# Kernel optimization log

Measured on AMD Instinct MI355X. Metric: run time of the kernel, lower is better.

Reference implementation:

```python
import jax, jax.numpy as jnp
import numpy as np

D_MODEL, D_K, D_V, N_HEADS = 1024, 64, 64, 16
B, S = 2, 2048
LN_EPS = 1e-5


def setup_inputs() -> dict:
    key = jax.random.key(0)
    ks = jax.random.split(key, 12)
    s = 1.0 / np.sqrt(D_MODEL)
    inp = {
        "Q": jax.random.normal(ks[0], (B, S, D_MODEL), jnp.float32),
        "K": jax.random.normal(ks[1], (B, S, D_MODEL), jnp.float32),
        "V": jax.random.normal(ks[2], (B, S, D_MODEL), jnp.float32),
        "attn_mask": jax.random.bernoulli(ks[3], 0.1, (B, S, S)),
        "Wq": jax.random.uniform(ks[4], (D_MODEL, D_K * N_HEADS), jnp.float32, -s, s),
        "bq": jnp.zeros((D_K * N_HEADS,), jnp.float32),
        "Wk": jax.random.uniform(ks[5], (D_MODEL, D_K * N_HEADS), jnp.float32, -s, s),
        "bk": jnp.zeros((D_K * N_HEADS,), jnp.float32),
        "Wv": jax.random.uniform(ks[6], (D_MODEL, D_V * N_HEADS), jnp.float32, -s, s),
        "bv": jnp.zeros((D_V * N_HEADS,), jnp.float32),
        "Wo": jax.random.uniform(ks[7], (N_HEADS * D_V, D_MODEL), jnp.float32, -s, s),
        "bo": jnp.zeros((D_MODEL,), jnp.float32),
        "gamma": jnp.ones((D_MODEL,), jnp.float32),
        "beta": jnp.zeros((D_MODEL,), jnp.float32),
    }
    return inp


def reference(Q, K, V, attn_mask, Wq, bq, Wk, bk, Wv, bv, Wo, bo, gamma, beta):
    b, s, _ = Q.shape
    # projections -> [B, S, H, d]
    q = (Q @ Wq + bq).reshape(b, s, N_HEADS, D_K)
    k = (K @ Wk + bk).reshape(b, -1, N_HEADS, D_K)
    v = (V @ Wv + bv).reshape(b, -1, N_HEADS, D_V)
    # scores [B, H, Sq, Sk]
    scores = jnp.einsum("bqhd,bkhd->bhqk", q, k) / np.sqrt(D_K).astype(np.float32)
    scores = jnp.where(attn_mask[:, None, :, :], jnp.float32(-1e9), scores)
    attn = jax.nn.softmax(scores, axis=-1)
    context = jnp.einsum("bhqk,bkhd->bqhd", attn, v).reshape(b, s, N_HEADS * D_V)
    out = context @ Wo + bo + Q  # residual
    mu = jnp.mean(out, axis=-1, keepdims=True)
    var = jnp.var(out, axis=-1, keepdims=True)
    return (out - mu) * jax.lax.rsqrt(var + LN_EPS) * gamma + beta
```

## Files before the change

kernel.cpp:

```cpp
#include <hip/hip_runtime.h>
#include <hip/hip_bf16.h>
#include <math.h>


#define D_MODEL 1024
#define NHEADS  16
#define DHEAD   64
#define BATCH   2
#define SEQ     2048
#define MROWS   (BATCH * SEQ)
#define SCLF    0.18033688f

typedef __attribute__((ext_vector_type(8)))  short bf16x8;
typedef __attribute__((ext_vector_type(4)))  float f32x4;
typedef __attribute__((ext_vector_type(16))) float f32x16;

__device__ inline unsigned short f2bf(float f) {
    unsigned int u = __builtin_bit_cast(unsigned int, f);
    unsigned int r = (u + 0x7FFFu + ((u >> 16) & 1u)) >> 16;
    return (unsigned short)r;
}

__device__ inline unsigned cvtpk_bf16(float lo, float hi2) {
    unsigned r;
    asm("v_cvt_pk_bf16_f32 %0, %1, %2" : "=v"(r) : "v"(lo), "v"(hi2));
    return r;
}

__device__ inline void gload16(const unsigned short* g, unsigned short* lbase, int lane) {
#if __has_builtin(__builtin_amdgcn_global_load_lds)
    __builtin_amdgcn_global_load_lds(
        (const __attribute__((address_space(1))) unsigned int*)g,
        (__attribute__((address_space(3))) unsigned int*)lbase, 16, 0, 0);
#else
    *(bf16x8*)(lbase + lane * 8) = *(const bf16x8*)g;
#endif
}

__global__ __launch_bounds__(256) void detect_mask_par(
    const unsigned int* __restrict__ m, int nwords, int* __restrict__ flags)
{
    const int i = blockIdx.x * 256 + threadIdx.x;
    int a = 0, b = 0;
    if (i < nwords) {
        const unsigned int w = m[i];
        a = (w != 0u && w != 1u);
        b = (w != 0u && w != 0x3F800000u);
    }
    const int wa = (int)__any(a);
    const int wb = (int)__any(b);
    if ((threadIdx.x & 63) == 0) {
        if (wa) atomicOr(&flags[0], 1);
        if (wb) atomicOr(&flags[1], 1);
    }
}

__global__ __launch_bounds__(256) void pack_mask_ballot(
    const void* __restrict__ mask, const int* __restrict__ flags,
    unsigned long long* __restrict__ mbits, int nwords)
{
    const int lane   = threadIdx.x & 63;
    const int wv     = blockIdx.x * 4 + (threadIdx.x >> 6);
    const int nwaves = gridDim.x * 4;
    const int mf = (flags[0] == 0) ? 0 : (flags[1] == 0) ? 1 : 2;
    for (int w = wv; w < nwords; w += nwaves) {
        bool bit;
        if (mf == 0)      bit = ((const unsigned int*)mask)[(size_t)w * 64 + lane] != 0u;
        else if (mf == 1) bit = ((const float*)mask)[(size_t)w * 64 + lane] != 0.f;
        else              bit = ((const unsigned char*)mask)[(size_t)w * 64 + lane] != 0;
        const unsigned long long b = __ballot(bit);
        if (lane == 0) mbits[w] = b;
    }
}

__global__ __launch_bounds__(256) void cvt_all(
    const float* __restrict__ Q, const float* __restrict__ K,
    const float* __restrict__ V,
    const float* __restrict__ w0, const float* __restrict__ w1,
    const float* __restrict__ w2, const float* __restrict__ w3,
    unsigned short* __restrict__ Qb, unsigned short* __restrict__ Kb,
    unsigned short* __restrict__ Vb,
    unsigned short* __restrict__ t0, unsigned short* __restrict__ t1,
    unsigned short* __restrict__ t2, unsigned short* __restrict__ t3)
{
    __shared__ float tile[64][65];
    const int z = blockIdx.z;
    if (z < 3) {
        const float* s = (z == 0) ? Q : (z == 1) ? K : V;
        unsigned short* d = (z == 0) ? Qb : (z == 1) ? Kb : Vb;
        const int i = blockIdx.x * 256 + threadIdx.x;
        float4 a = ((const float4*)s)[i * 2];
        float4 b = ((const float4*)s)[i * 2 + 1];
        unsigned u0 = cvtpk_bf16(a.x, a.y);
        unsigned u1 = cvtpk_bf16(a.z, a.w);
        unsigned u2 = cvtpk_bf16(b.x, b.y);
        unsigned u3 = cvtpk_bf16(b.z, b.w);
        ((int4*)d)[i] = make_int4((int)u0, (int)u1, (int)u2, (int)u3);
    } else {
        if (blockIdx.x >= 256) return;
        const int wz = z - 3;
        const float* W = (wz == 0) ? w0 : (wz == 1) ? w1 : (wz == 2) ? w2 : w3;
        unsigned short* T = (wz == 0) ? t0 : (wz == 1) ? t1 : (wz == 2) ? t2 : t3;
        const int n0 = (blockIdx.x & 15) * 64;
        const int k0 = (blockIdx.x >> 4) * 64;
        const int t  = threadIdx.x;
        const int r  = t >> 4;
        const int c4 = (t & 15) * 4;
        #pragma unroll
        for (int u = 0; u < 4; ++u) {
            float4 v = *(const float4*)(W + (size_t)(k0 + r + u * 16) * D_MODEL + n0 + c4);
            tile[r + u * 16][c4 + 0] = v.x;
            tile[r + u * 16][c4 + 1] = v.y;
            tile[r + u * 16][c4 + 2] = v.z;
            tile[r + u * 16][c4 + 3] = v.w;
        }
        __syncthreads();
        #pragma unroll
        for (int u = 0; u < 4; ++u) {
            const int nr = r + u * 16;
            ushort4 o;
            o.x = f2bf(tile[c4 + 0][nr]);
            o.y = f2bf(tile[c4 + 1][nr]);
            o.z = f2bf(tile[c4 + 2][nr]);
            o.w = f2bf(tile[c4 + 3][nr]);
            *(ushort4*)(T + (size_t)(n0 + nr) * D_MODEL + k0 + c4) = o;
        }
    }
}

#define BKQ 32
__global__ __launch_bounds__(256, 1) void gemm_qkv(
    const unsigned short* __restrict__ A0, const unsigned short* __restrict__ A1,
    const unsigned short* __restrict__ A2,
    const unsigned short* __restrict__ B0, const unsigned short* __restrict__ B1,
    const unsigned short* __restrict__ B2,
    const float* __restrict__ bias0, const float* __restrict__ bias1,
    const float* __restrict__ bias2,
    unsigned short* __restrict__ C0, unsigned short* __restrict__ C1,
    unsigned short* __restrict__ C2)
{
    const int z = blockIdx.z;
    const unsigned short* A  = (z == 0) ? A0 : (z == 1) ? A1 : A2;
    const unsigned short* Bt = (z == 0) ? B0 : (z == 1) ? B1 : B2;
    const float* bias        = (z == 0) ? bias0 : (z == 1) ? bias1 : bias2;
    unsigned short* C        = (z == 0) ? C0 : (z == 1) ? C1 : C2;
    const int K = D_MODEL, N = D_MODEL;

    __shared__ unsigned short As[2][128 * BKQ];
    __shared__ unsigned short Bs[2][128 * BKQ];
    const int tid  = threadIdx.x;
    const int w    = tid >> 6;
    const int lane = tid & 63;
    const int lo   = lane & 15;
    const int hi   = lane >> 4;
    const int wm   = (w >> 1) * 64;
    const int wn   = (w & 1) * 64;
    const int m0   = blockIdx.x * 128;
    const int n0   = blockIdx.y * 128;

    const unsigned short* Ab = A  + (size_t)m0 * K;
    const unsigned short* Bb = Bt + (size_t)n0 * K;

    f32x4 acc[4][4];
    #pragma unroll
    for (int i = 0; i < 4; ++i)
        #pragma unroll
        for (int j = 0; j < 4; ++j) acc[i][j] = (f32x4){0.f, 0.f, 0.f, 0.f};

    const int NT = K / BKQ;
    auto stage = [&](int buf, int t) {
        const int k0 = t * BKQ;
        #pragma unroll
        for (int i = 0; i < 2; ++i) {
            const int c = i * 256 + tid;
            gload16(Ab + (size_t)(c >> 2) * K + k0 + (c & 3) * 8,
                    &As[buf][(i * 256 + w * 64) * 8], lane);
        }
        #pragma unroll
        for (int i = 0; i < 2; ++i) {
            const int c = i * 256 + tid;
            gload16(Bb + (size_t)(c >> 2) * K + k0 + (c & 3) * 8,
                    &Bs[buf][(i * 256 + w * 64) * 8], lane);
        }
    };

    stage(0, 0);
    __syncthreads();
    int cur = 0;
    for (int t = 0; t < NT; ++t) {
        if (t + 1 < NT) stage(cur ^ 1, t + 1);
        bf16x8 af[4], bfr[4];
        #pragma unroll
        for (int f = 0; f < 4; ++f) {
            af[f]  = *(const bf16x8*)&As[cur][(wm + f * 16 + lo) * BKQ + hi * 8];
            bfr[f] = *(const bf16x8*)&Bs[cur][(wn + f * 16 + lo) * BKQ + hi * 8];
        }
        #pragma unroll
        for (int fm = 0; fm < 4; ++fm)
            #pragma unroll
            for (int fn = 0; fn < 4; ++fn)
                acc[fm][fn] = __builtin_amdgcn_mfma_f32_16x16x32_bf16(
                    af[fm], bfr[fn], acc[fm][fn], 0, 0, 0);
        __syncthreads();
        cur ^= 1;
    }

    #pragma unroll
    for (int fm = 0; fm < 4; ++fm) {
        const int row = m0 + wm + fm * 16 + hi * 4;
        #pragma unroll
        for (int fn = 0; fn < 4; ++fn) {
            const int col = n0 + wn + fn * 16 + lo;
            const float bv = bias[col];
            #pragma unroll
            for (int r = 0; r < 4; ++r) {
                float o = acc[fm][fn][r] + bv;
                if (z == 0) o *= SCLF;
                if (z < 2)
                    C[(size_t)(row + r) * N + col] = f2bf(o);
                else
                    C[(size_t)((row + r) >> 11) * 2097152
                      + (size_t)col * 2048 + ((row + r) & 2047)] = f2bf(o);
            }
        }
    }
}

#define BKK 64
__global__ __launch_bounds__(256) void gemm_out64(
    const unsigned short* __restrict__ A, const unsigned short* __restrict__ Bt,
    const float* __restrict__ bias, const float* __restrict__ resid,
    float* __restrict__ C)
{
    const int K = D_MODEL, N = D_MODEL;
    __shared__ unsigned short As[2][128 * BKK];
    __shared__ unsigned short Bs[2][64 * BKK];
    const int tid  = threadIdx.x;
    const int w    = tid >> 6;
    const int lane = tid & 63;
    const int lo   = lane & 15;
    const int hi   = lane >> 4;
    const int wm   = (w >> 1) * 64;
    const int wn   = (w & 1) * 32;
    const int m0   = blockIdx.x * 128;
    const int n0   = blockIdx.y * 64;

    const unsigned short* Ab = A  + (size_t)m0 * K;
    const unsigned short* Bb = Bt + (size_t)n0 * K;

    f32x4 acc[4][2];
    #pragma unroll
    for (int i = 0; i < 4; ++i)
        #pragma unroll
        for (int j = 0; j < 2; ++j) acc[i][j] = (f32x4){0.f, 0.f, 0.f, 0.f};

    const int NT = K / BKK;
    auto stage = [&](int buf, int t) {
        const int k0 = t * BKK;
        #pragma unroll
        for (int i = 0; i < 4; ++i) {
            const int c = i * 256 + tid;
            gload16(Ab + (size_t)(c >> 3) * K + k0 + (c & 7) * 8,
                    &As[buf][(i * 256 + w * 64) * 8], lane);
        }
        #pragma unroll
        for (int i = 0; i < 2; ++i) {
            const int c = i * 256 + tid;
            gload16(Bb + (size_t)(c >> 3) * K + k0 + (c & 7) * 8,
                    &Bs[buf][(i * 256 + w * 64) * 8], lane);
        }
    };

    stage(0, 0);
    __syncthreads();
    int cur = 0;
    for (int t = 0; t < NT; ++t) {
        if (t + 1 < NT) stage(cur ^ 1, t + 1);
        bf16x8 af[4][2], bfr[2][2];
        #pragma unroll
        for (int f = 0; f < 4; ++f)
            #pragma unroll
            for (int s = 0; s < 2; ++s)
                af[f][s] = *(const bf16x8*)&As[cur][(wm + f * 16 + lo) * BKK + s * 32 + hi * 8];
        #pragma unroll
        for (int f = 0; f < 2; ++f)
            #pragma unroll
            for (int s = 0; s < 2; ++s)
                bfr[f][s] = *(const bf16x8*)&Bs[cur][(wn + f * 16 + lo) * BKK + s * 32 + hi * 8];
        #pragma unroll
        for (int s = 0; s < 2; ++s)
            #pragma unroll
            for (int fm = 0; fm < 4; ++fm)
                #pragma unroll
                for (int fn = 0; fn < 2; ++fn)
                    acc[fm][fn] = __builtin_amdgcn_mfma_f32_16x16x32_bf16(
                        af[fm][s], bfr[fn][s], acc[fm][fn], 0, 0, 0);
        __syncthreads();
        cur ^= 1;
    }

    #pragma unroll
    for (int fm = 0; fm < 4; ++fm) {
        const int row = m0 + wm + fm * 16 + hi * 4;
        #pragma unroll
        for (int fn = 0; fn < 2; ++fn) {
            const int col = n0 + wn + fn * 16 + lo;
            const float bv = bias[col];
            #pragma unroll
            for (int r = 0; r < 4; ++r)
                C[(size_t)(row + r) * N + col] =
                    acc[fm][fn][r] + bv + resid[(size_t)(row + r) * N + col];
        }
    }
}

__global__ __launch_bounds__(512, 2) void attn_mfma32(
    const unsigned short* __restrict__ qb, const unsigned short* __restrict__ kbm,
    const unsigned short* __restrict__ vt,
    const unsigned long long* __restrict__ mbits, unsigned short* __restrict__ ctx)
{
    __shared__ unsigned char smem[65536];
    const int tid  = threadIdx.x;
    const int w8   = tid >> 6;
    const int g    = w8 >> 2;
    const int wq   = w8 & 3;
    const int lane = tid & 63;
    const int l31  = lane & 31;
    const int hi   = lane >> 5;
    const int h    = blockIdx.x;
    const int q0   = blockIdx.y * 128;
    const int b    = blockIdx.z;

    unsigned short* KsG = (unsigned short*)smem + (size_t)g * 8192;
    unsigned short* VsG = (unsigned short*)(smem + 32768) + (size_t)g * 8192;

    const size_t qkbase = (size_t)b * SEQ * D_MODEL + (size_t)h * DHEAD;
    const size_t vtbase = ((size_t)b * D_MODEL + h * DHEAD) * SEQ;

    const int qtok = q0 + wq * 32 + l31;
    bf16x8 qA[4];
    #pragma unroll
    for (int s = 0; s < 4; ++s)
        qA[s] = *(const bf16x8*)(qb + qkbase + (size_t)qtok * D_MODEL + s * 16 + hi * 8);

    f32x16 o0 = {}, o1 = {};
    float l_i = 0.f;

    const unsigned long long* mrow = mbits + ((size_t)b * SEQ + qtok) * (SEQ / 64);

    const int srow = lane >> 3;
    const int sc   = lane & 7;
    const int r0   = wq * 16 + srow;
    const int swz  = sc ^ (r0 & 7);

    const unsigned short* kl0 = kbm + qkbase + (size_t)(g * 1024 + r0) * D_MODEL + swz * 8;
    const unsigned short* kl1 = kl0 + (size_t)8 * D_MODEL;
    const unsigned short* vl0 = vt + vtbase + (size_t)r0 * SEQ + g * 1024 + swz * 8;
    const unsigned short* vl1 = vl0 + (size_t)8 * SEQ;
    const int ldk0 = (wq * 16) * 64;
    const int ldk1 = (wq * 16 + 8) * 64;

    auto stage = [&](int buf) {
        gload16(kl0, &KsG[buf * 4096 + ldk0], lane);
        gload16(kl1, &KsG[buf * 4096 + ldk1], lane);
        gload16(vl0, &VsG[buf * 4096 + ldk0], lane);
        gload16(vl1, &VsG[buf * 4096 + ldk1], lane);
        kl0 += (size_t)64 * D_MODEL;
        kl1 += (size_t)64 * D_MODEL;
        vl0 += 64;
        vl1 += 64;
    };

    stage(0);
    unsigned long long mw64 = mrow[g * 16];
    __syncthreads();
    int cur = 0;

    for (int t = 0; t < 16; ++t) {
        if (t + 1 < 16) stage(cur ^ 1);
        const unsigned long long mwc = mw64;
        if (t + 1 < 16) mw64 = mrow[g * 16 + t + 1];
        const unsigned int ml = (unsigned int)(mwc >> (4 * hi));
        const unsigned int mh = (unsigned int)(mwc >> (32 + 4 * hi));

        f32x16 st0 = {}, st1 = {};
        __builtin_amdgcn_s_setprio(1);
        #pragma unroll
        for (int s = 0; s < 4; ++s) {
            bf16x8 kf0 = *(const bf16x8*)&KsG[cur * 4096 + l31 * 64 + ((2 * s + hi) ^ (l31 & 7)) * 8];
            st0 = __builtin_amdgcn_mfma_f32_32x32x16_bf16(kf0, qA[s], st0, 0, 0, 0);
            bf16x8 kf1 = *(const bf16x8*)&KsG[cur * 4096 + (32 + l31) * 64 + ((2 * s + hi) ^ (l31 & 7)) * 8];
            st1 = __builtin_amdgcn_mfma_f32_32x32x16_bf16(kf1, qA[s], st1, 0, 0, 0);
        }
        __builtin_amdgcn_s_setprio(0);

        float sp[4] = {0.f, 0.f, 0.f, 0.f};
        #pragma unroll
        for (int r = 0; r < 16; ++r) {
            const int klo = (r & 3) + 8 * (r >> 2);
            const float x0 = ((ml >> klo) & 1u) ? -1e9f : st0[r];
            const float x1 = ((mh >> klo) & 1u) ? -1e9f : st1[r];
            const float e0 = exp2f(x0);
            const float e1 = exp2f(x1);
            st0[r] = e0; st1[r] = e1;
            sp[r & 3] += e0 + e1;
        }
        l_i += (sp[0] + sp[1]) + (sp[2] + sp[3]);

        bf16x8 pa[4];
        #pragma unroll
        for (int s = 0; s < 4; ++s) {
            const int base = (s & 1) * 8;
            unsigned av, bv2, cv, dv;
            if (s < 2) {
                av  = cvtpk_bf16(st0[base + 0], st0[base + 1]);
                bv2 = cvtpk_bf16(st0[base + 4], st0[base + 5]);
                cv  = cvtpk_bf16(st0[base + 2], st0[base + 3]);
                dv  = cvtpk_bf16(st0[base + 6], st0[base + 7]);
            } else {
                av  = cvtpk_bf16(st1[base + 0], st1[base + 1]);
                bv2 = cvtpk_bf16(st1[base + 4], st1[base + 5]);
                cv  = cvtpk_bf16(st1[base + 2], st1[base + 3]);
                dv  = cvtpk_bf16(st1[base + 6], st1[base + 7]);
            }
            asm("v_permlane32_swap_b32 %0, %1" : "+v"(av), "+v"(bv2));
            asm("v_permlane32_swap_b32 %0, %1" : "+v"(cv), "+v"(dv));
            int4 pk = make_int4((int)av, (int)cv, (int)bv2, (int)dv);
            pa[s] = __builtin_bit_cast(bf16x8, pk);
        }

        __builtin_amdgcn_s_setprio(1);
        #pragma unroll
        for (int s = 0; s < 4; ++s) {
            bf16x8 vf0 = *(const bf16x8*)&VsG[cur * 4096 + l31 * 64 + ((2 * s + hi) ^ (l31 & 7)) * 8];
            o0 = __builtin_amdgcn_mfma_f32_32x32x16_bf16(pa[s], vf0, o0, 0, 0, 0);
            bf16x8 vf1 = *(const bf16x8*)&VsG[cur * 4096 + (32 + l31) * 64 + ((2 * s + hi) ^ (l31 & 7)) * 8];
            o1 = __builtin_amdgcn_mfma_f32_32x32x16_bf16(pa[s], vf1, o1, 0, 0, 0);
        }
        __builtin_amdgcn_s_setprio(0);
        __syncthreads();
        cur ^= 1;
    }

    l_i += __shfl_xor(l_i, 32, 64);
    __syncthreads();
    float* comb = (float*)smem;
    if (g == 1) {
        float* p = comb + (size_t)(wq * 64 + lane) * 33;
        #pragma unroll
        for (int r = 0; r < 16; ++r) { p[r] = o0[r]; p[16 + r] = o1[r]; }
        p[32] = l_i;
    }
    __syncthreads();
    if (g == 0) {
        const float* p = comb + (size_t)(wq * 64 + lane) * 33;
        const float inv = 1.f / (l_i + p[32]);
        #pragma unroll
        for (int r = 0; r < 16; ++r) {
            const int qloc = (r & 3) + 8 * (r >> 2) + 4 * hi;
            const float ivr = __shfl(inv, qloc, 64);
            unsigned short* dst = ctx + qkbase + (size_t)(q0 + wq * 32 + qloc) * D_MODEL;
            dst[l31]      = f2bf((o0[r] + p[r]) * ivr);
            dst[32 + l31] = f2bf((o1[r] + p[16 + r]) * ivr);
        }
    }
}

__global__ __launch_bounds__(256) void layernorm1024(
    const float* __restrict__ x, const float* __restrict__ gamma,
    const float* __restrict__ beta, float* __restrict__ out)
{
    const int row = blockIdx.x;
    const int tid = threadIdx.x;
    const float* xr = x + (size_t)row * D_MODEL;
    float4 v = *(const float4*)(xr + (tid << 2));
    float s = v.x + v.y + v.z + v.w;
    float q = v.x * v.x + v.y * v.y + v.z * v.z + v.w * v.w;
    #pragma unroll
    for (int off = 1; off < 64; off <<= 1) {
        s += __shfl_xor(s, off, 64);
        q += __shfl_xor(q, off, 64);
    }
    __shared__ float sw[4], qw_[4];
    const int wid = tid >> 6;
    if ((tid & 63) == 0) { sw[wid] = s; qw_[wid] = q; }
    __syncthreads();
    s = sw[0] + sw[1] + sw[2] + sw[3];
    q = qw_[0] + qw_[1] + qw_[2] + qw_[3];
    const float mu  = s * (1.f / D_MODEL);
    const float var = q * (1.f / D_MODEL) - mu * mu;
    const float a = var + 1e-5f;
    float inv = rsqrtf(a);
    inv = inv * (1.5f - 0.5f * a * inv * inv);
    float4 gg = *(const float4*)(gamma + (tid << 2));
    float4 bt = *(const float4*)(beta + (tid << 2));
    float4 o;
    o.x = (v.x - mu) * inv * gg.x + bt.x;
    o.y = (v.y - mu) * inv * gg.y + bt.y;
    o.z = (v.z - mu) * inv * gg.z + bt.z;
    o.w = (v.w - mu) * inv * gg.w + bt.w;
    *(float4*)(out + (size_t)row * D_MODEL + (tid << 2)) = o;
}

extern "C" void kernel_launch(void* const* d_in, const int* in_sizes, int n_in,
                              void* d_out, int out_size, void* d_ws, size_t ws_size,
                              hipStream_t stream)
{
    const float* Q    = (const float*)d_in[0];
    const float* K    = (const float*)d_in[1];
    const float* V    = (const float*)d_in[2];
    const void*  mask = d_in[3];
    const float* Wq   = (const float*)d_in[4];
    const float* bq   = (const float*)d_in[5];
    const float* Wk   = (const float*)d_in[6];
    const float* bk   = (const float*)d_in[7];
    const float* Wv   = (const float*)d_in[8];
    const float* bv   = (const float*)d_in[9];
    const float* Wo   = (const float*)d_in[10];
    const float* bo   = (const float*)d_in[11];
    const float* gam  = (const float*)d_in[12];
    const float* bet  = (const float*)d_in[13];
    float* out = (float*)d_out;

    const size_t NE = (size_t)MROWS * D_MODEL;
    const size_t WE = (size_t)D_MODEL * D_MODEL;
    const size_t NMW = (size_t)BATCH * SEQ * (SEQ / 64);
    unsigned short* Qbf = (unsigned short*)d_ws;
    unsigned short* Kbf = Qbf + NE;
    unsigned short* Vbf = Kbf + NE;
    unsigned short* qb  = Vbf + NE;
    unsigned short* kb  = qb + NE;
    unsigned short* vt  = kb + NE;
    unsigned short* Wt0 = vt + NE;
    unsigned short* Wt1 = Wt0 + WE;
    unsigned short* Wt2 = Wt1 + WE;
    unsigned short* Wt3 = Wt2 + WE;
    unsigned long long* mbits = (unsigned long long*)(Wt3 + WE);
    int* mflags = (int*)(mbits + NMW);
    unsigned short* ctxb = Qbf;
    float* outp = (float*)Kbf;
    if (ws_size < 6 * NE * 2 + 4 * WE * 2 + NMW * 8 + 64) return;

    hipMemsetAsync(mflags, 0, 2 * sizeof(int), stream);
    detect_mask_par<<<256, 256, 0, stream>>>((const unsigned int*)mask, 65536, mflags);
    pack_mask_ballot<<<2048, 256, 0, stream>>>(mask, mflags, mbits, (int)NMW);

    cvt_all<<<dim3(2048, 1, 7), 256, 0, stream>>>(Q, K, V, Wq, Wk, Wv, Wo,
                                                  Qbf, Kbf, Vbf, Wt0, Wt1, Wt2, Wt3);

    gemm_qkv<<<dim3(32, 8, 3), 256, 0, stream>>>(Qbf, Kbf, Vbf, Wt0, Wt1, Wt2,
                                                 bq, bk, bv, qb, kb, vt);

    dim3 ag(NHEADS, SEQ / 128, BATCH);
    attn_mfma32<<<ag, 512, 0, stream>>>(qb, kb, vt, mbits, ctxb);

    gemm_out64<<<dim3(32, 16), 256, 0, stream>>>(ctxb, Wt3, bo, Q, outp);

    layernorm1024<<<MROWS, 256, 0, stream>>>(outp, gam, bet, out);
}
```

Before: 187.3 us.

## Halve attention KV tile to 32 keys to shrink LDS and registers

Cuts the per-iteration key/value tile in the attention kernel from 64 to 32 keys, doubling the loop trip count. Shared memory drops from 64KB to about 33KB, and the score accumulators and P fragments are halved. The K and V staging layouts and swizzles are reworked to fit the smaller tile. This is meant to lower LDS and register pressure so more blocks can be resident, at the cost of twice as many barriers and stage steps per pass with less MFMA work between them.

```diff
diff --git a/kernel.cpp b/kernel.cpp
--- a/kernel.cpp
+++ b/kernel.cpp
@@ -319,7 +319,7 @@
     const unsigned short* __restrict__ vt,
     const unsigned long long* __restrict__ mbits, unsigned short* __restrict__ ctx)
 {
-    __shared__ unsigned char smem[65536];
+    __shared__ __align__(16) unsigned char smem[33792];
     const int tid  = threadIdx.x;
     const int w8   = tid >> 6;
     const int g    = w8 >> 2;
@@ -331,8 +331,8 @@
     const int q0   = blockIdx.y * 128;
     const int b    = blockIdx.z;
 
-    unsigned short* KsG = (unsigned short*)smem + (size_t)g * 8192;
-    unsigned short* VsG = (unsigned short*)(smem + 32768) + (size_t)g * 8192;
+    unsigned short* KsG = (unsigned short*)smem + (size_t)g * 4096;
+    unsigned short* VsG = (unsigned short*)(smem + 16384) + (size_t)g * 4096;
 
     const size_t qkbase = (size_t)b * SEQ * D_MODEL + (size_t)h * DHEAD;
     const size_t vtbase = ((size_t)b * D_MODEL + h * DHEAD) * SEQ;
@@ -348,27 +348,22 @@
 
     const unsigned long long* mrow = mbits + ((size_t)b * SEQ + qtok) * (SEQ / 64);
 
-    const int srow = lane >> 3;
-    const int sc   = lane & 7;
-    const int r0   = wq * 16 + srow;
-    const int swz  = sc ^ (r0 & 7);
-
-    const unsigned short* kl0 = kbm + qkbase + (size_t)(g * 1024 + r0) * D_MODEL + swz * 8;
-    const unsigned short* kl1 = kl0 + (size_t)8 * D_MODEL;
-    const unsigned short* vl0 = vt + vtbase + (size_t)r0 * SEQ + g * 1024 + swz * 8;
-    const unsigned short* vl1 = vl0 + (size_t)8 * SEQ;
-    const int ldk0 = (wq * 16) * 64;
-    const int ldk1 = (wq * 16 + 8) * 64;
+    const int krow = wq * 8 + (lane >> 3);
+    const int kc   = lane & 7;
+    const int kswz = kc ^ (krow & 7);
+    const int vrow = wq * 16 + (lane >> 2);
+    const int vsrc = ((lane & 3) - vrow) & 3;
+
+    const unsigned short* kl = kbm + qkbase + (size_t)(g * 1024 + krow) * D_MODEL + kswz * 8;
+    const unsigned short* vl = vt + vtbase + (size_t)vrow * SEQ + g * 1024 + vsrc * 8;
+    const int kldb = (wq * 8) * 64;
+    const int vldb = (wq * 16) * 32;
 
     auto stage = [&](int buf) {
-        gload16(kl0, &KsG[buf * 4096 + ldk0], lane);
-        gload16(kl1, &KsG[buf * 4096 + ldk1], lane);
-        gload16(vl0, &VsG[buf * 4096 + ldk0], lane);
-        gload16(vl1, &VsG[buf * 4096 + ldk1], lane);
-        kl0 += (size_t)64 * D_MODEL;
-        kl1 += (size_t)64 * D_MODEL;
-        vl0 += 64;
-        vl1 += 64;
+        gload16(kl, &KsG[buf * 2048 + kldb], lane);
+        gload16(vl, &VsG[buf * 2048 + vldb], lane);
+        kl += (size_t)32 * D_MODEL;
+        vl += 32;
     };
 
     stage(0);
@@ -376,21 +371,17 @@
     __syncthreads();
     int cur = 0;
 
-    for (int t = 0; t < 16; ++t) {
-        if (t + 1 < 16) stage(cur ^ 1);
-        const unsigned long long mwc = mw64;
-        if (t + 1 < 16) mw64 = mrow[g * 16 + t + 1];
-        const unsigned int ml = (unsigned int)(mwc >> (4 * hi));
-        const unsigned int mh = (unsigned int)(mwc >> (32 + 4 * hi));
-
-        f32x16 st0 = {}, st1 = {};
+    for (int t = 0; t < 32; ++t) {
+        if (t + 1 < 32) stage(cur ^ 1);
+        const unsigned int mw = (unsigned int)(mw64 >> (32 * (t & 1) + 4 * hi));
+        if ((t & 1) && t + 1 < 32) mw64 = mrow[g * 16 + ((t + 1) >> 1)];
+
+        f32x16 st = {};
         __builtin_amdgcn_s_setprio(1);
         #pragma unroll
         for (int s = 0; s < 4; ++s) {
-            bf16x8 kf0 = *(const bf16x8*)&KsG[cur * 4096 + l31 * 64 + ((2 * s + hi) ^ (l31 & 7)) * 8];
-            st0 = __builtin_amdgcn_mfma_f32_32x32x16_bf16(kf0, qA[s], st0, 0, 0, 0);
-            bf16x8 kf1 = *(const bf16x8*)&KsG[cur * 4096 + (32 + l31) * 64 + ((2 * s + hi) ^ (l31 & 7)) * 8];
-            st1 = __builtin_amdgcn_mfma_f32_32x32x16_bf16(kf1, qA[s], st1, 0, 0, 0);
+            bf16x8 kf = *(const bf16x8*)&KsG[cur * 2048 + l31 * 64 + ((2 * s + hi) ^ (l31 & 7)) * 8];
+            st = __builtin_amdgcn_mfma_f32_32x32x16_bf16(kf, qA[s], st, 0, 0, 0);
         }
         __builtin_amdgcn_s_setprio(0);
 
@@ -398,31 +389,21 @@
         #pragma unroll
         for (int r = 0; r < 16; ++r) {
             const int klo = (r & 3) + 8 * (r >> 2);
-            const float x0 = ((ml >> klo) & 1u) ? -1e9f : st0[r];
-            const float x1 = ((mh >> klo) & 1u) ? -1e9f : st1[r];
-            const float e0 = exp2f(x0);
-            const float e1 = exp2f(x1);
-            st0[r] = e0; st1[r] = e1;
-            sp[r & 3] += e0 + e1;
+            const float x = ((mw >> klo) & 1u) ? -1e9f : st[r];
+            const float e = exp2f(x);
+            st[r] = e;
+            sp[r & 3] += e;
         }
         l_i += (sp[0] + sp[1]) + (sp[2] + sp[3]);
 
-        bf16x8 pa[4];
-        #pragma unroll
-        for (int s = 0; s < 4; ++s) {
-            const int base = (s & 1) * 8;
-            unsigned av, bv2, cv, dv;
-            if (s < 2) {
-                av  = cvtpk_bf16(st0[base + 0], st0[base + 1]);
-                bv2 = cvtpk_bf16(st0[base + 4], st0[base + 5]);
-                cv  = cvtpk_bf16(st0[base + 2], st0[base + 3]);
-                dv  = cvtpk_bf16(st0[base + 6], st0[base + 7]);
-            } else {
-                av  = cvtpk_bf16(st1[base + 0], st1[base + 1]);
-                bv2 = cvtpk_bf16(st1[base + 4], st1[base + 5]);
-                cv  = cvtpk_bf16(st1[base + 2], st1[base + 3]);
-                dv  = cvtpk_bf16(st1[base + 6], st1[base + 7]);
-            }
+        bf16x8 pa[2];
+        #pragma unroll
+        for (int s = 0; s < 2; ++s) {
+            const int base = s * 8;
+            unsigned av  = cvtpk_bf16(st[base + 0], st[base + 1]);
+            unsigned bv2 = cvtpk_bf16(st[base + 4], st[base + 5]);
+            unsigned cv  = cvtpk_bf16(st[base + 2], st[base + 3]);
+            unsigned dv  = cvtpk_bf16(st[base + 6], st[base + 7]);
             asm("v_permlane32_swap_b32 %0, %1" : "+v"(av), "+v"(bv2));
             asm("v_permlane32_swap_b32 %0, %1" : "+v"(cv), "+v"(dv));
             int4 pk = make_int4((int)av, (int)cv, (int)bv2, (int)dv);
@@ -431,10 +412,11 @@
 
         __builtin_amdgcn_s_setprio(1);
         #pragma unroll
-        for (int s = 0; s < 4; ++s) {
-            bf16x8 vf0 = *(const bf16x8*)&VsG[cur * 4096 + l31 * 64 + ((2 * s + hi) ^ (l31 & 7)) * 8];
+        for (int s = 0; s < 2; ++s) {
+            const int slot = ((2 * s + hi) + l31) & 3;
+            bf16x8 vf0 = *(const bf16x8*)&VsG[cur * 2048 + l31 * 32 + slot * 8];
             o0 = __builtin_amdgcn_mfma_f32_32x32x16_bf16(pa[s], vf0, o0, 0, 0, 0);
-            bf16x8 vf1 = *(const bf16x8*)&VsG[cur * 4096 + (32 + l31) * 64 + ((2 * s + hi) ^ (l31 & 7)) * 8];
+            bf16x8 vf1 = *(const bf16x8*)&VsG[cur * 2048 + (32 + l31) * 32 + slot * 8];
             o1 = __builtin_amdgcn_mfma_f32_32x32x16_bf16(pa[s], vf1, o1, 0, 0, 0);
         }
         __builtin_amdgcn_s_setprio(0);
```

Result: faster. 180.9 us (-3.5%).
